# Kernel optimization log

Hardware: AMD Instinct MI355X
Metric: run time of the kernel (lower is better)

The kernel has to match this reference:

```python
import jax, jax.numpy as jnp
import numpy as np

SIG = 0.5
EPSILON = 10.0
E = float(np.e)


def setup_inputs() -> dict:
    key = jax.random.key(0)
    k1, k2, k3, k4 = jax.random.split(key, 4)
    B, S, D, K = 8, 2048, 128, 64
    features = jax.random.normal(k1, (B, S, D), dtype=jnp.float32)
    centroids = jax.random.normal(k2, (K, D), dtype=jnp.float32)
    # phi are per-class scale stats; keep strictly positive
    phi = jax.random.uniform(k3, (K,), dtype=jnp.float32, minval=0.5, maxval=1.5)
    labels = jax.random.randint(k4, (B, S), 0, K, dtype=jnp.int32)
    return {"features": features, "centroids": centroids, "phi": phi, "labels": labels}


def _proto_supcon_loss(features, centroids, phi, labels):
    B, S, D = features.shape
    K = centroids.shape[0]
    # pairwise mean-squared-error (MSELoss reduction='mean' over D):
    # d2[b,i,j] = mean_d (f[b,i,d]-f[b,j,d])^2
    sq = jnp.sum(features * features, axis=-1)  # [B,S]
    gram = jnp.einsum('bid,bjd->bij', features, features)  # [B,S,S]
    d2 = (sq[:, :, None] + sq[:, None, :] - 2.0 * gram) / D
    d2 = jnp.maximum(d2, 0.0)

    same = labels[:, :, None] == labels[:, None, :]  # [B,S,S]
    neg_mask = ~same
    neg_cnt = jnp.sum(neg_mask, axis=-1)  # [B,S]
    # negative sample term: neg_x = mean over negatives of MSE; neg_sup = x*log(x+e)
    neg_x = jnp.sum(jnp.where(neg_mask, d2, 0.0), axis=-1) / jnp.maximum(neg_cnt, 1)
    neg_sup = neg_x * jnp.log(neg_x + E)

    # positive sample term: mean over same-label j != i (0 if no other positive,
    # matching pos_dis = [0] in the original)
    eye = jnp.eye(S, dtype=bool)
    pos_mask = same & ~eye
    pos_cnt = jnp.sum(pos_mask, axis=-1)
    pos_x = jnp.sum(jnp.where(pos_mask, d2, 0.0), axis=-1) / jnp.maximum(pos_cnt, 1)

    # centroid terms: MSE(feature, centroid_k)/phi_k, [B,S,K]
    csq = jnp.sum(centroids * centroids, axis=-1)  # [K]
    cgram = jnp.einsum('bsd,kd->bsk', features, centroids)
    cd2 = (sq[:, :, None] + csq[None, None, :] - 2.0 * cgram) / D
    cd2 = jnp.maximum(cd2, 0.0) / phi[None, None, :]

    pos_cent = jnp.take_along_axis(cd2, labels[:, :, None].astype(jnp.int32), axis=2)[..., 0]  # [B,S]
    neg_cent_x = (jnp.sum(cd2, axis=-1) - pos_cent) / (K - 1)
    neg_cent_log = neg_cent_x * jnp.log(neg_cent_x + E)

    pos_spcl = SIG * pos_x + (1.0 - SIG) * pos_cent
    neg_spcl = SIG * neg_sup + (1.0 - SIG) * neg_cent_log
    per_anchor = pos_spcl - neg_spcl + EPSILON

    # anchors contribute only if they have at least one negative sample
    contrib = neg_cnt > 0
    loss = jnp.sum(jnp.where(contrib, per_anchor, 0.0)) / S
    return loss.reshape(1, 1)


def reference(features, centroids, phi, labels):
    return _proto_supcon_loss(features, centroids, phi, labels)
```

## Files before the change

kernel.cpp:

```cpp
#include <hip/hip_runtime.h>
#include <math.h>

#define B_ 8
#define S_ 2048
#define D_ 128
#define K_ 64
#define SIG_ 0.5f
#define EPS_ 10.0f
#define E_ 2.718281828459045f

__device__ __forceinline__ int remap512(int bx) { return ((bx & 7) << 6) | (bx >> 3); }
__device__ __forceinline__ int remap256(int bx) { return ((bx & 7) << 5) | (bx >> 3); }

__global__ void __launch_bounds__(256) k1_stats(
    const float* __restrict__ F, const float* __restrict__ C,
    const int* __restrict__ L,
    float* __restrict__ fsumK, float* __restrict__ ssumK, float* __restrict__ cntK,
    float* __restrict__ csqK) {
    int bx = remap512(blockIdx.x);
    int k = bx & (K_ - 1);
    int b = bx >> 6;
    int tid = threadIdx.x;
    int lane = tid & 63;
    int wv = tid >> 6;

    __shared__ float redF[4][128];
    __shared__ float redS[4];
    __shared__ int   redC[4];

    const int* Lb = L + b * S_;
    const float* Fb = F + (size_t)b * S_ * D_;

    float a0 = 0.f, a1 = 0.f, q0 = 0.f, q1 = 0.f;
    int cnt = 0;
    #pragma unroll
    for (int rr = 0; rr < 8; ++rr) {
        int r = (wv << 3) + rr;
        int lbl = Lb[(r << 6) + lane];
        unsigned long long m = __ballot(lbl == k);
        cnt += (int)__popcll(m);
        while (m) {
            int i = __ffsll((long long)m) - 1;
            m &= m - 1;
            const float* row = Fb + (size_t)((r << 6) + i) * D_;
            float v0 = row[lane];
            float v1 = row[64 + lane];
            a0 += v0; q0 = fmaf(v0, v0, q0);
            a1 += v1; q1 = fmaf(v1, v1, q1);
        }
    }
    float qq = q0 + q1;
    #pragma unroll
    for (int m = 1; m < 64; m <<= 1) qq += __shfl_xor(qq, m);
    redF[wv][lane] = a0;
    redF[wv][64 + lane] = a1;
    if (lane == 0) { redS[wv] = qq; redC[wv] = cnt; }
    __syncthreads();

    if (tid < 128) {
        float s = (redF[0][tid] + redF[1][tid]) + (redF[2][tid] + redF[3][tid]);
        fsumK[(size_t)bx * D_ + tid] = s;
    }
    if (tid == 0) {
        ssumK[bx] = (redS[0] + redS[1]) + (redS[2] + redS[3]);
        cntK[bx] = (float)(redC[0] + redC[1] + redC[2] + redC[3]);
    }
    if (b == 0 && wv == 0) {
        float x0 = C[(k << 7) + lane];
        float x1 = C[(k << 7) + 64 + lane];
        float cs = fmaf(x0, x0, x1 * x1);
        #pragma unroll
        for (int m = 1; m < 64; m <<= 1) cs += __shfl_xor(cs, m);
        if (lane == 0) csqK[k] = cs;
    }
}

__global__ void __launch_bounds__(512) k3_main(
    const float* __restrict__ F, const float* __restrict__ C,
    const float* __restrict__ phi, const int* __restrict__ L,
    const float* __restrict__ fsumK, const float* __restrict__ ssumK,
    const float* __restrict__ cntK, const float* __restrict__ csqK,
    float* __restrict__ partial) {

    __shared__ float Cs[K_ * 129];
    __shared__ float Ft[64 * D_];
    __shared__ float4 redA[256];
    __shared__ float Fa[D_];
    __shared__ float wacc[8];
    int tid = threadIdx.x;
    int bxw = remap256(blockIdx.x);
    int b = bxw >> 5;

    {
        const float4* C4 = (const float4*)C;
        #pragma unroll
        for (int it = 0; it < 4; ++it) {
            int i = it * 512 + tid;
            float4 v = C4[i];
            float* p = &Cs[(i >> 5) * 129 + ((i & 31) << 2)];
            p[0] = v.x; p[1] = v.y; p[2] = v.z; p[3] = v.w;
        }
    }
    {
        const float4* Fb4 = (const float4*)(F + (size_t)(bxw * 64) * D_);
        float4* Ft4 = (float4*)Ft;
        #pragma unroll
        for (int it = 0; it < 4; ++it) {
            int i = it * 512 + tid;
            Ft4[i] = Fb4[i];
        }
    }
    if (tid < 256) {
        int d4 = tid & 31, kg = tid >> 5;
        const float4* g4 = (const float4*)(fsumK + (size_t)b * K_ * D_) + (size_t)kg * 8 * 32 + d4;
        float4 s; s.x = s.y = s.z = s.w = 0.f;
        #pragma unroll
        for (int kk = 0; kk < 8; ++kk) {
            float4 v = g4[(size_t)kk * 32];
            s.x += v.x; s.y += v.y; s.z += v.z; s.w += v.w;
        }
        redA[tid] = s;
    }
    __syncthreads();
    if (tid < 32) {
        float4 a; a.x = a.y = a.z = a.w = 0.f;
        #pragma unroll
        for (int g = 0; g < 8; ++g) {
            float4 v = redA[g * 32 + tid];
            a.x += v.x; a.y += v.y; a.z += v.z; a.w += v.w;
        }
        ((float4*)Fa)[tid] = a;
    }
    __syncthreads();

    int lane = tid & 63;

    float csq = csqK[lane];
    float phv = phi[lane];
    float ssl = ssumK[b * K_ + lane];
    float cnl = cntK[b * K_ + lane];
    float ssA = ssl;
    #pragma unroll
    for (int m = 1; m < 64; m <<= 1) ssA += __shfl_xor(ssA, m);

    int wid = __builtin_amdgcn_readfirstlane(tid) >> 6;
    int a0g = bxw * 64 + wid * 8;
    int j_of = lane >> 3, q = lane & 7;
    int lbl_p = L[a0g + j_of];
    const float4* frL = (const float4*)(Ft + (wid * 8 + j_of) * D_);
    const float4* fk = (const float4*)(fsumK + (size_t)(b * K_ + lbl_p) * D_);
    const float4* fa4 = (const float4*)Fa;

    float sq_p = 0.f, dk_p = 0.f, da_p = 0.f;
    #pragma unroll
    for (int i = 0; i < 4; ++i) {
        int dq = i * 8 + q;
        float4 fv = frL[dq];
        float4 kv = fk[dq];
        float4 av = fa4[dq];
        sq_p = fmaf(fv.x, fv.x, fmaf(fv.y, fv.y, fmaf(fv.z, fv.z, fmaf(fv.w, fv.w, sq_p))));
        dk_p = fmaf(fv.x, kv.x, fmaf(fv.y, kv.y, fmaf(fv.z, kv.z, fmaf(fv.w, kv.w, dk_p))));
        da_p = fmaf(fv.x, av.x, fmaf(fv.y, av.y, fmaf(fv.z, av.z, fmaf(fv.w, av.w, da_p))));
    }
    #pragma unroll
    for (int m = 1; m < 8; m <<= 1) {
        sq_p += __shfl_xor(sq_p, m);
        dk_p += __shfl_xor(dk_p, m);
        da_p += __shfl_xor(da_p, m);
    }

    const float4* FtW = (const float4*)(Ft + (wid * 8) * D_);
    float facc[8];
    #pragma unroll
    for (int j = 0; j < 8; ++j) facc[j] = 0.f;

    for (int dq = 0; dq < 32; ++dq) {
        int cbase = lane * 129 + (dq << 2);
        float cv0 = Cs[cbase + 0];
        float cv1 = Cs[cbase + 1];
        float cv2 = Cs[cbase + 2];
        float cv3 = Cs[cbase + 3];
        #pragma unroll
        for (int j = 0; j < 8; ++j) {
            float4 fb = FtW[j * 32 + dq];
            facc[j] = fmaf(fb.x, cv0, fmaf(fb.y, cv1,
                      fmaf(fb.z, cv2, fmaf(fb.w, cv3, facc[j]))));
        }
    }

    float acc = 0.f;
    #pragma unroll
    for (int j = 0; j < 8; ++j) {
        float sq_j = __shfl(sq_p, j * 8);
        float dk_j = __shfl(dk_p, j * 8);
        float da_j = __shfl(da_p, j * 8);
        int lbl_j = __shfl(lbl_p, j * 8);
        float cnt_j = __shfl(cnl, lbl_j);
        float ssm_j = __shfl(ssl, lbl_j);

        float cd2 = (sq_j + csq - 2.f * facc[j]) * (1.f / D_);
        cd2 = fmaxf(cd2, 0.f) / phv;

        float s_cd = cd2;
        #pragma unroll
        for (int m = 1; m < 64; m <<= 1) s_cd += __shfl_xor(s_cd, m);
        float pos_cent = __shfl(cd2, lbl_j);

        float ncx = (s_cd - pos_cent) * (1.f / (K_ - 1));
        float S_same = (cnt_j * sq_j + ssm_j - 2.f * dk_j) * (1.f / D_);
        float S_all = ((float)S_ * sq_j + ssA - 2.f * da_j) * (1.f / D_);
        float pos_x = fmaxf(S_same, 0.f) / fmaxf(cnt_j - 1.f, 1.f);
        float neg_cnt = (float)S_ - cnt_j;
        float neg_x = fmaxf(S_all - S_same, 0.f) / fmaxf(neg_cnt, 1.f);

        float neg_sup = neg_x * __logf(neg_x + E_);
        float ncl = ncx * __logf(ncx + E_);

        float pa = SIG_ * pos_x + (1.f - SIG_) * pos_cent
                 - (SIG_ * neg_sup + (1.f - SIG_) * ncl) + EPS_;
        if (neg_cnt > 0.5f) acc += pa;
    }

    if (lane == 0) wacc[wid] = acc;
    __syncthreads();

    if (tid == 0) {
        float s = 0.f;
        #pragma unroll
        for (int w = 0; w < 8; ++w) s += wacc[w];
        partial[bxw] = s;
    }
}

__global__ void __launch_bounds__(256) k4_reduce(
    const float* __restrict__ partial, float* __restrict__ out) {
    int tid = threadIdx.x;
    int lane = tid & 63;
    int wv = tid >> 6;
    __shared__ float w[4];
    float v = partial[tid];
    #pragma unroll
    for (int m = 1; m < 64; m <<= 1) v += __shfl_xor(v, m);
    if (lane == 0) w[wv] = v;
    __syncthreads();
    if (tid == 0) out[0] = (w[0] + w[1] + w[2] + w[3]) * (1.0f / (float)S_);
}

extern "C" void kernel_launch(void* const* d_in, const int* in_sizes, int n_in,
                              void* d_out, int out_size, void* d_ws, size_t ws_size,
                              hipStream_t stream) {
    const float* F = (const float*)d_in[0];
    const float* C = (const float*)d_in[1];
    const float* phi = (const float*)d_in[2];
    const int* L = (const int*)d_in[3];
    float* out = (float*)d_out;

    float* ws = (float*)d_ws;
    float* fsumK = ws;
    float* ssumK = fsumK + (size_t)B_ * K_ * D_;
    float* cntK  = ssumK + B_ * K_;
    float* csqK  = cntK + B_ * K_;
    float* partial = csqK + K_;

    k1_stats<<<B_ * K_, 256, 0, stream>>>(F, C, L, fsumK, ssumK, cntK, csqK);
    k3_main<<<256, 512, 0, stream>>>(F, C, phi, L, fsumK, ssumK, cntK, csqK, partial);
    k4_reduce<<<1, 256, 0, stream>>>(partial, out);
}
```

Baseline: 24.87 us.

## Run centroid distance work concurrently with per-class stats in one fused kernel

Splits the work so that the per-class statistics and the feature-centroid distance computation (which does not depend on those stats) run as two disjoint block groups in a single launch. The centroid results (row norm, sum of distances, positive distance) go to a small workspace buffer, and a lighter post kernel combines them with the class stats. Centroid norms are now computed in-block rather than in the stats kernel. The aim is to overlap the ballot-driven stats pass with the heavy centroid matmul and shorten the critical path. In exchange, the fused kernel holds the large shared-memory footprint for all its blocks, which may limit occupancy for the stats half, and there is an extra global round-trip through the workspace.

```diff
diff --git a/kernel.cpp b/kernel.cpp
--- a/kernel.cpp
+++ b/kernel.cpp
@@ -9,81 +9,161 @@
 #define EPS_ 10.0f
 #define E_ 2.718281828459045f
 
-__device__ __forceinline__ int remap512(int bx) { return ((bx & 7) << 6) | (bx >> 3); }
 __device__ __forceinline__ int remap256(int bx) { return ((bx & 7) << 5) | (bx >> 3); }
 
-__global__ void __launch_bounds__(256) k1_stats(
-    const float* __restrict__ F, const float* __restrict__ C,
-    const int* __restrict__ L,
-    float* __restrict__ fsumK, float* __restrict__ ssumK, float* __restrict__ cntK,
-    float* __restrict__ csqK) {
-    int bx = remap512(blockIdx.x);
-    int k = bx & (K_ - 1);
-    int b = bx >> 6;
-    int tid = threadIdx.x;
-    int lane = tid & 63;
-    int wv = tid >> 6;
-
-    __shared__ float redF[4][128];
-    __shared__ float redS[4];
-    __shared__ int   redC[4];
-
-    const int* Lb = L + b * S_;
-    const float* Fb = F + (size_t)b * S_ * D_;
-
-    float a0 = 0.f, a1 = 0.f, q0 = 0.f, q1 = 0.f;
-    int cnt = 0;
-    #pragma unroll
-    for (int rr = 0; rr < 8; ++rr) {
-        int r = (wv << 3) + rr;
-        int lbl = Lb[(r << 6) + lane];
-        unsigned long long m = __ballot(lbl == k);
-        cnt += (int)__popcll(m);
-        while (m) {
-            int i = __ffsll((long long)m) - 1;
-            m &= m - 1;
-            const float* row = Fb + (size_t)((r << 6) + i) * D_;
-            float v0 = row[lane];
-            float v1 = row[64 + lane];
-            a0 += v0; q0 = fmaf(v0, v0, q0);
-            a1 += v1; q1 = fmaf(v1, v1, q1);
-        }
-    }
-    float qq = q0 + q1;
-    #pragma unroll
-    for (int m = 1; m < 64; m <<= 1) qq += __shfl_xor(qq, m);
-    redF[wv][lane] = a0;
-    redF[wv][64 + lane] = a1;
-    if (lane == 0) { redS[wv] = qq; redC[wv] = cnt; }
-    __syncthreads();
-
-    if (tid < 128) {
-        float s = (redF[0][tid] + redF[1][tid]) + (redF[2][tid] + redF[3][tid]);
-        fsumK[(size_t)bx * D_ + tid] = s;
-    }
-    if (tid == 0) {
-        ssumK[bx] = (redS[0] + redS[1]) + (redS[2] + redS[3]);
-        cntK[bx] = (float)(redC[0] + redC[1] + redC[2] + redC[3]);
-    }
-    if (b == 0 && wv == 0) {
-        float x0 = C[(k << 7) + lane];
-        float x1 = C[(k << 7) + 64 + lane];
-        float cs = fmaf(x0, x0, x1 * x1);
-        #pragma unroll
-        for (int m = 1; m < 64; m <<= 1) cs += __shfl_xor(cs, m);
-        if (lane == 0) csqK[k] = cs;
-    }
-}
-
-__global__ void __launch_bounds__(512) k3_main(
+__global__ void __launch_bounds__(512) fused1(
     const float* __restrict__ F, const float* __restrict__ C,
     const float* __restrict__ phi, const int* __restrict__ L,
+    float* __restrict__ fsumK, float* __restrict__ ssumK, float* __restrict__ cntK,
+    float* __restrict__ pre) {
+
+    int tid = threadIdx.x;
+
+    if (blockIdx.x < 256) {
+        __shared__ float Cs[K_ * 129];
+        __shared__ float Ft[64 * D_];
+        __shared__ float csqS[K_];
+        int bxw = remap256(blockIdx.x);
+
+        {
+            const float4* C4 = (const float4*)C;
+            #pragma unroll
+            for (int it = 0; it < 4; ++it) {
+                int i = it * 512 + tid;
+                float4 v = C4[i];
+                float* p = &Cs[(i >> 5) * 129 + ((i & 31) << 2)];
+                p[0] = v.x; p[1] = v.y; p[2] = v.z; p[3] = v.w;
+                float d2 = fmaf(v.x, v.x, fmaf(v.y, v.y, fmaf(v.z, v.z, v.w * v.w)));
+                #pragma unroll
+                for (int m = 1; m < 32; m <<= 1) d2 += __shfl_xor(d2, m);
+                if ((tid & 31) == 0) csqS[i >> 5] = d2;
+            }
+        }
+        {
+            const float4* Fb4 = (const float4*)(F + (size_t)(bxw * 64) * D_);
+            float4* Ft4 = (float4*)Ft;
+            #pragma unroll
+            for (int it = 0; it < 4; ++it) {
+                int i = it * 512 + tid;
+                Ft4[i] = Fb4[i];
+            }
+        }
+        __syncthreads();
+
+        int lane = tid & 63;
+        int wid = __builtin_amdgcn_readfirstlane(tid) >> 6;
+        float csq = csqS[lane];
+        float phv = phi[lane];
+        int a0g = bxw * 64 + wid * 8;
+
+        const float4* FtW = (const float4*)(Ft + (wid * 8) * D_);
+        float facc[8];
+        #pragma unroll
+        for (int j = 0; j < 8; ++j) facc[j] = 0.f;
+        for (int dq = 0; dq < 32; ++dq) {
+            int cbase = lane * 129 + (dq << 2);
+            float cv0 = Cs[cbase + 0];
+            float cv1 = Cs[cbase + 1];
+            float cv2 = Cs[cbase + 2];
+            float cv3 = Cs[cbase + 3];
+            #pragma unroll
+            for (int j = 0; j < 8; ++j) {
+                float4 fb = FtW[j * 32 + dq];
+                facc[j] = fmaf(fb.x, cv0, fmaf(fb.y, cv1,
+                          fmaf(fb.z, cv2, fmaf(fb.w, cv3, facc[j]))));
+            }
+        }
+
+        int j_of = lane >> 3, q = lane & 7;
+        const float4* frL = (const float4*)(Ft + (wid * 8 + j_of) * D_);
+        float sq_p = 0.f;
+        #pragma unroll
+        for (int i = 0; i < 4; ++i) {
+            float4 fv = frL[i * 8 + q];
+            sq_p = fmaf(fv.x, fv.x, fmaf(fv.y, fv.y, fmaf(fv.z, fv.z, fmaf(fv.w, fv.w, sq_p))));
+        }
+        #pragma unroll
+        for (int m = 1; m < 8; m <<= 1) sq_p += __shfl_xor(sq_p, m);
+
+        int lbl_p = L[a0g + j_of];
+
+        #pragma unroll
+        for (int j = 0; j < 8; ++j) {
+            float sq_j = __shfl(sq_p, j * 8);
+            int lbl_j = __shfl(lbl_p, j * 8);
+            float cd2 = (sq_j + csq - 2.f * facc[j]) * (1.f / D_);
+            cd2 = fmaxf(cd2, 0.f) / phv;
+            float s_cd = cd2;
+            #pragma unroll
+            for (int m = 1; m < 64; m <<= 1) s_cd += __shfl_xor(s_cd, m);
+            float pc = __shfl(cd2, lbl_j);
+            if (lane == 0) {
+                float* pp = pre + (size_t)(a0g + j) * 3;
+                pp[0] = sq_j; pp[1] = s_cd; pp[2] = pc;
+            }
+        }
+    } else {
+        __shared__ float redF[2][4][128];
+        __shared__ float redS[2][4];
+        __shared__ int   redC[2][4];
+        int jb = blockIdx.x - 256;
+        int b = jb & 7;
+        int cp = jb >> 3;
+        int lane = tid & 63;
+        int wv = tid >> 6;
+        int g = wv >> 2;
+        int k = cp * 2 + g;
+        int wg = wv & 3;
+
+        const int* Lb = L + b * S_;
+        const float* Fb = F + (size_t)b * S_ * D_;
+
+        float a0 = 0.f, a1 = 0.f, q0 = 0.f, q1 = 0.f;
+        int cnt = 0;
+        #pragma unroll
+        for (int rr = 0; rr < 8; ++rr) {
+            int r = (wg << 3) + rr;
+            int lbl = Lb[(r << 6) + lane];
+            unsigned long long m = __ballot(lbl == k);
+            cnt += (int)__popcll(m);
+            while (m) {
+                int i = __ffsll((long long)m) - 1;
+                m &= m - 1;
+                const float* row = Fb + (size_t)((r << 6) + i) * D_;
+                float v0 = row[lane];
+                float v1 = row[64 + lane];
+                a0 += v0; q0 = fmaf(v0, v0, q0);
+                a1 += v1; q1 = fmaf(v1, v1, q1);
+            }
+        }
+        float qq = q0 + q1;
+        #pragma unroll
+        for (int m = 1; m < 64; m <<= 1) qq += __shfl_xor(qq, m);
+        redF[g][wg][lane] = a0;
+        redF[g][wg][64 + lane] = a1;
+        if (lane == 0) { redS[g][wg] = qq; redC[g][wg] = cnt; }
+        __syncthreads();
+
+        if (tid < 256) {
+            int g2 = tid >> 7, d = tid & 127;
+            float s = (redF[g2][0][d] + redF[g2][1][d]) + (redF[g2][2][d] + redF[g2][3][d]);
+            fsumK[(size_t)(b * K_ + cp * 2 + g2) * D_ + d] = s;
+            if (d == 0) {
+                ssumK[b * K_ + cp * 2 + g2] =
+                    (redS[g2][0] + redS[g2][1]) + (redS[g2][2] + redS[g2][3]);
+                cntK[b * K_ + cp * 2 + g2] =
+                    (float)(redC[g2][0] + redC[g2][1] + redC[g2][2] + redC[g2][3]);
+            }
+        }
+    }
+}
+
+__global__ void __launch_bounds__(512) k_post(
+    const float* __restrict__ F, const int* __restrict__ L,
     const float* __restrict__ fsumK, const float* __restrict__ ssumK,
-    const float* __restrict__ cntK, const float* __restrict__ csqK,
+    const float* __restrict__ cntK, const float* __restrict__ pre,
     float* __restrict__ partial) {
 
-    __shared__ float Cs[K_ * 129];
-    __shared__ float Ft[64 * D_];
     __shared__ float4 redA[256];
     __shared__ float Fa[D_];
     __shared__ float wacc[8];
@@ -91,25 +171,6 @@
     int bxw = remap256(blockIdx.x);
     int b = bxw >> 5;
 
-    {
-        const float4* C4 = (const float4*)C;
-        #pragma unroll
-        for (int it = 0; it < 4; ++it) {
-            int i = it * 512 + tid;
-            float4 v = C4[i];
-            float* p = &Cs[(i >> 5) * 129 + ((i & 31) << 2)];
-            p[0] = v.x; p[1] = v.y; p[2] = v.z; p[3] = v.w;
-        }
-    }
-    {
-        const float4* Fb4 = (const float4*)(F + (size_t)(bxw * 64) * D_);
-        float4* Ft4 = (float4*)Ft;
-        #pragma unroll
-        for (int it = 0; it < 4; ++it) {
-            int i = it * 512 + tid;
-            Ft4[i] = Fb4[i];
-        }
-    }
     if (tid < 256) {
         int d4 = tid & 31, kg = tid >> 5;
         const float4* g4 = (const float4*)(fsumK + (size_t)b * K_ * D_) + (size_t)kg * 8 * 32 + d4;
@@ -134,9 +195,6 @@
     __syncthreads();
 
     int lane = tid & 63;
-
-    float csq = csqK[lane];
-    float phv = phi[lane];
     float ssl = ssumK[b * K_ + lane];
     float cnl = cntK[b * K_ + lane];
     float ssA = ssl;
@@ -145,68 +203,46 @@
 
     int wid = __builtin_amdgcn_readfirstlane(tid) >> 6;
     int a0g = bxw * 64 + wid * 8;
+    const float4* F4 = (const float4*)F;
+
     int j_of = lane >> 3, q = lane & 7;
-    int lbl_p = L[a0g + j_of];
-    const float4* frL = (const float4*)(Ft + (wid * 8 + j_of) * D_);
+    int a_mine = a0g + j_of;
+    int lbl_p = L[a_mine];
+    const float4* fr = F4 + (size_t)a_mine * 32;
     const float4* fk = (const float4*)(fsumK + (size_t)(b * K_ + lbl_p) * D_);
     const float4* fa4 = (const float4*)Fa;
 
-    float sq_p = 0.f, dk_p = 0.f, da_p = 0.f;
+    float dk_p = 0.f, da_p = 0.f;
     #pragma unroll
     for (int i = 0; i < 4; ++i) {
         int dq = i * 8 + q;
-        float4 fv = frL[dq];
+        float4 fv = fr[dq];
         float4 kv = fk[dq];
         float4 av = fa4[dq];
-        sq_p = fmaf(fv.x, fv.x, fmaf(fv.y, fv.y, fmaf(fv.z, fv.z, fmaf(fv.w, fv.w, sq_p))));
         dk_p = fmaf(fv.x, kv.x, fmaf(fv.y, kv.y, fmaf(fv.z, kv.z, fmaf(fv.w, kv.w, dk_p))));
         da_p = fmaf(fv.x, av.x, fmaf(fv.y, av.y, fmaf(fv.z, av.z, fmaf(fv.w, av.w, da_p))));
     }
     #pragma unroll
     for (int m = 1; m < 8; m <<= 1) {
-        sq_p += __shfl_xor(sq_p, m);
         dk_p += __shfl_xor(dk_p, m);
         da_p += __shfl_xor(da_p, m);
     }
 
-    const float4* FtW = (const float4*)(Ft + (wid * 8) * D_);
-    float facc[8];
-    #pragma unroll
-    for (int j = 0; j < 8; ++j) facc[j] = 0.f;
-
-    for (int dq = 0; dq < 32; ++dq) {
-        int cbase = lane * 129 + (dq << 2);
-        float cv0 = Cs[cbase + 0];
-        float cv1 = Cs[cbase + 1];
-        float cv2 = Cs[cbase + 2];
-        float cv3 = Cs[cbase + 3];
-        #pragma unroll
-        for (int j = 0; j < 8; ++j) {
-            float4 fb = FtW[j * 32 + dq];
-            facc[j] = fmaf(fb.x, cv0, fmaf(fb.y, cv1,
-                      fmaf(fb.z, cv2, fmaf(fb.w, cv3, facc[j]))));
-        }
-    }
+    float prev = (lane < 24) ? pre[(size_t)a0g * 3 + lane] : 0.f;
 
     float acc = 0.f;
     #pragma unroll
     for (int j = 0; j < 8; ++j) {
-        float sq_j = __shfl(sq_p, j * 8);
+        float sq_j  = __shfl(prev, j * 3 + 0);
+        float scd_j = __shfl(prev, j * 3 + 1);
+        float pc_j  = __shfl(prev, j * 3 + 2);
         float dk_j = __shfl(dk_p, j * 8);
         float da_j = __shfl(da_p, j * 8);
         int lbl_j = __shfl(lbl_p, j * 8);
         float cnt_j = __shfl(cnl, lbl_j);
         float ssm_j = __shfl(ssl, lbl_j);
 
-        float cd2 = (sq_j + csq - 2.f * facc[j]) * (1.f / D_);
-        cd2 = fmaxf(cd2, 0.f) / phv;
-
-        float s_cd = cd2;
-        #pragma unroll
-        for (int m = 1; m < 64; m <<= 1) s_cd += __shfl_xor(s_cd, m);
-        float pos_cent = __shfl(cd2, lbl_j);
-
-        float ncx = (s_cd - pos_cent) * (1.f / (K_ - 1));
+        float ncx = (scd_j - pc_j) * (1.f / (K_ - 1));
         float S_same = (cnt_j * sq_j + ssm_j - 2.f * dk_j) * (1.f / D_);
         float S_all = ((float)S_ * sq_j + ssA - 2.f * da_j) * (1.f / D_);
         float pos_x = fmaxf(S_same, 0.f) / fmaxf(cnt_j - 1.f, 1.f);
@@ -216,7 +252,7 @@
         float neg_sup = neg_x * __logf(neg_x + E_);
         float ncl = ncx * __logf(ncx + E_);
 
-        float pa = SIG_ * pos_x + (1.f - SIG_) * pos_cent
+        float pa = SIG_ * pos_x + (1.f - SIG_) * pc_j
                  - (SIG_ * neg_sup + (1.f - SIG_) * ncl) + EPS_;
         if (neg_cnt > 0.5f) acc += pa;
     }
@@ -259,10 +295,10 @@
     float* fsumK = ws;
     float* ssumK = fsumK + (size_t)B_ * K_ * D_;
     float* cntK  = ssumK + B_ * K_;
-    float* csqK  = cntK + B_ * K_;
-    float* partial = csqK + K_;
-
-    k1_stats<<<B_ * K_, 256, 0, stream>>>(F, C, L, fsumK, ssumK, cntK, csqK);
-    k3_main<<<256, 512, 0, stream>>>(F, C, phi, L, fsumK, ssumK, cntK, csqK, partial);
+    float* partial = cntK + B_ * K_;
+    float* pre = partial + 256;
+
+    fused1<<<512, 512, 0, stream>>>(F, C, phi, L, fsumK, ssumK, cntK, pre);
+    k_post<<<256, 512, 0, stream>>>(F, L, fsumK, ssumK, cntK, pre, partial);
     k4_reduce<<<1, 256, 0, stream>>>(partial, out);
 }
```

New measurement: 23.70 us (median of 2 runs). -4.7%, faster.
